# Kernel optimization log

Hardware: AMD Instinct MI355X
Metric: run time of the kernel (lower is better)

## Reference

```python
import jax, jax.numpy as jnp
import numpy as np

CONF = 0.25      # confidence threshold (module default)
IOU = 0.45       # NMS IoU threshold (class attribute)
TOPK = 1000      # fixed candidate budget (jit-friendly stand-in for boolean filtering)
MAX_WH = 4096.0  # class offset so NMS is per-class (YOLOv5 trick)


def xywh2xyxy(b):
    xy, wh = b[..., :2], b[..., 2:4]
    return jnp.concatenate([xy - wh * 0.5, xy + wh * 0.5], axis=-1)


def box_iou(a, b):
    # a: [K,4] xyxy, b: [K,4] xyxy -> [K,K]
    lt = jnp.maximum(a[:, None, :2], b[None, :, :2])
    rb = jnp.minimum(a[:, None, 2:], b[None, :, 2:])
    wh = jnp.clip(rb - lt, 0.0)
    inter = wh[..., 0] * wh[..., 1]
    area_a = (a[:, 2] - a[:, 0]) * (a[:, 3] - a[:, 1])
    area_b = (b[:, 2] - b[:, 0]) * (b[:, 3] - b[:, 1])
    return inter / (area_a[:, None] + area_b[None, :] - inter + 1e-9)


def nms_single(pred):
    # pred: [N, 5+C] = (xywh, obj, cls scores)
    boxes = xywh2xyxy(pred[:, :4])
    obj = pred[:, 4]
    cls = pred[:, 5:]
    cls_conf = jnp.max(cls, axis=-1)
    cls_id = jnp.argmax(cls, axis=-1)
    score = obj * cls_conf                       # conf = obj_conf * cls_conf
    masked = jnp.where(score > CONF, score, -1.0)
    top_scores, idx = jax.lax.top_k(masked, TOPK)  # sorted descending
    boxes_k = boxes[idx]                          # [K,4]
    cls_k = cls_id[idx].astype(boxes.dtype)       # [K]
    valid_k = top_scores > CONF                   # candidates passing threshold
    # per-class NMS via coordinate offset
    off = boxes_k + cls_k[:, None] * MAX_WH
    iou = box_iou(off, off)
    iou = iou * (1.0 - jnp.eye(TOPK, dtype=iou.dtype))  # ignore self-IoU
    # greedy suppression in descending score order
    def step(suppressed, i):
        keep_i = jnp.logical_and(jnp.logical_not(suppressed[i]), valid_k[i])
        suppressed = jnp.logical_or(suppressed, jnp.logical_and(keep_i, iou[i] > IOU))
        return suppressed, keep_i
    _, keep = jax.lax.scan(step, jnp.zeros(TOPK, dtype=bool), jnp.arange(TOPK))
    det = jnp.concatenate([boxes_k, top_scores[:, None], cls_k[:, None]], axis=-1)  # [K,6]
    return jnp.where(keep[:, None], det, 0.0)


def setup_inputs() -> dict:
    key = jax.random.key(0)
    x = jax.random.uniform(key, (8, 25200, 85), dtype=jnp.float32)
    return {"x": x}


def reference(x):
    # [B, K, 6] detections (xyxy, conf, cls); suppressed/invalid rows zeroed.
    return jax.vmap(nms_single)(x)
```

## Files before the change

### kernel.cpp

```cpp
#include <hip/hip_runtime.h>
#include <stdint.h>

#define NB 8
#define NPRED 25200
#define NTOP 1000
#define NCLS 80
#define CONF_T 0.25f
#define IOU_THR 0.45f
#define MAXWH 4096.0f
#define CAP 2048
#define NBINS 1025
#define SBLK 128
#define SBPB 197

typedef unsigned long long u64;

__device__ __forceinline__ u64 shfl_xor_u64(u64 v, int m) {
    int lo = __shfl_xor((int)(unsigned)v, m);
    int hi = __shfl_xor((int)(unsigned)(v >> 32), m);
    return ((u64)(unsigned)hi << 32) | (unsigned)lo;
}

__global__ __launch_bounds__(256) void k_score(const float* __restrict__ x,
                                               float* __restrict__ msc,
                                               int* __restrict__ cls) {
#pragma clang fp contract(off)
    __shared__ __align__(16) float sm[SBLK * 85];
    const int b = blockIdx.x / SBPB;
    const int blk = blockIdx.x % SBPB;
    const int t = threadIdx.x;
    const int wave = t >> 6, lane = t & 63;
    const long long TOT4 = (long long)NB * NPRED * 85 / 4;
    const long long base4 = ((long long)b * NPRED + (long long)blk * SBLK) * 85 / 4;
    const float4* x4 = (const float4*)x;
    const int tile4 = SBLK * 85 / 4;

    for (int k = 0; k < 11; ++k) {
        int ib = k * 256 + wave * 64;
        int fi = ib + lane;
        if (fi < tile4) {
            long long gi = base4 + fi;
            if (gi >= TOT4) gi = TOT4 - 1;
            __builtin_amdgcn_global_load_lds(
                (const __attribute__((address_space(1))) void*)(x4 + gi),
                (__attribute__((address_space(3))) void*)(sm + (size_t)ib * 4),
                16, 0, 0);
        }
    }
    __syncthreads();

    const int p = t >> 1;
    const int h = t & 1;
    const int pred = blk * SBLK + p;
    const float* rowp = &sm[p * 85];
    float obj = rowp[4];
    const int cb = 5 + h * 40;
    float best = rowp[cb];
    int bid = h * 40;
    for (int c = 1; c < 40; ++c) {
        float v = rowp[cb + c];
        if (v > best) { best = v; bid = h * 40 + c; }
    }
    float obest = __shfl_xor(best, 1);
    int obid = __shfl_xor(bid, 1);
    if (h == 0 && pred < NPRED) {
        float fb = best; int fc = bid;
        if (obest > fb) { fb = obest; fc = obid; }
        float score = obj * fb;
        int q = b * NPRED + pred;
        msc[q] = (score > CONF_T) ? score : -1.0f;
        cls[q] = fc;
    }
}

__global__ __launch_bounds__(1024) void k_fused(const float* __restrict__ x,
                                                const float* __restrict__ msc,
                                                const int* __restrict__ cls,
                                                float* __restrict__ out) {
#pragma clang fp contract(off)
    __shared__ __align__(16) unsigned char uni[CAP * 8];
    __shared__ unsigned hh[NBINS];
    __shared__ __align__(16) float4 obx[NTOP];
    __shared__ float oco[NTOP];
    __shared__ float osc[NTOP];
    __shared__ int   ocl[NTOP];
    __shared__ int sB;
    __shared__ unsigned lcnt;
    __shared__ int ovf;
    u64* keys = (u64*)uni;
    const int b = blockIdx.x, t = threadIdx.x;
    const float* ms = msc + (size_t)b * NPRED;

    float sv[25];
#pragma unroll
    for (int k = 0; k < 25; ++k) {
        int p = t + k * 1024;
        sv[k] = (p < NPRED) ? ms[p] : -1.0f;
    }

    for (int i = t; i < NBINS; i += 1024) hh[i] = 0;
    if (t == 0) { lcnt = 0; ovf = 0; }
    __syncthreads();

#pragma unroll
    for (int k = 0; k < 25; ++k) {
        float s = sv[k];
        if (s > CONF_T) {
            unsigned bits = __float_as_uint(s);
            int bin = (int)(bits >> 14) - 0xFA00;
            bin = bin < 0 ? 0 : (bin > 1024 ? 1024 : bin);
            atomicAdd(&hh[bin], 1u);
        }
    }
    __syncthreads();

    if (t < 64) {
        const int lane = t;
        const int hi2 = 1024 - 16 * lane;
        unsigned sum = 0;
        for (int k = 0; k < 16; ++k) sum += hh[hi2 - k];
        if (lane == 63) sum += hh[0];
        unsigned v = sum;
        for (int d = 1; d < 64; d <<= 1) {
            unsigned o = __shfl_up(v, d);
            if (lane >= d) v += o;
        }
        unsigned excl = v - sum;
        u64 ball = __ballot(v >= NTOP);
        int B = 0;
        if (ball != 0) {
            int sel = __builtin_ctzll(ball);
            if (lane == sel) {
                unsigned run = excl;
                for (int k = 0; k < 16; ++k) {
                    run += hh[hi2 - k];
                    if (run >= NTOP) { B = hi2 - k; break; }
                }
            }
            B = __shfl(B, sel);
        }
        if (lane == 0) sB = B;
    }
    __syncthreads();
    const int B = sB;

#pragma unroll
    for (int k = 0; k < 25; ++k) {
        float s = sv[k];
        if (s > CONF_T) {
            unsigned bits = __float_as_uint(s);
            int bin = (int)(bits >> 14) - 0xFA00;
            bin = bin < 0 ? 0 : (bin > 1024 ? 1024 : bin);
            if (bin >= B) {
                unsigned slot = atomicAdd(&lcnt, 1u);
                if (slot < CAP)
                    keys[slot] = ((u64)(~bits) << 32) | (unsigned)(t + k * 1024);
            }
        }
    }
    __syncthreads();
    unsigned c = lcnt; if (c > CAP) c = CAP;
    for (int i = (int)c + t; i < CAP; i += 1024) keys[i] = ~0ULL;
    __syncthreads();

    const unsigned ia = (((unsigned)t & ~63u) << 1) | ((unsigned)t & 63u);
    const unsigned ib = ia + 64u;

    auto ce = [&](u64& v, unsigned i, unsigned j, unsigned k) {
        u64 pv = shfl_xor_u64(v, (int)j);
        bool asc = ((i & k) == 0u);
        bool lower = ((i & j) == 0u);
        bool takeMin = (asc == lower);
        bool less = (v < pv);
        v = (takeMin == less) ? v : pv;
    };

    {
        u64 a = keys[ia], d = keys[ib];
        for (unsigned k = 2; k <= 64; k <<= 1)
            for (unsigned j = k >> 1; j >= 1; j >>= 1) {
                ce(a, ia, j, k);
                ce(d, ib, j, k);
            }
        keys[ia] = a; keys[ib] = d;
    }
    __syncthreads();

    for (unsigned k = 128; k <= CAP; k <<= 1) {
        for (unsigned j = k >> 1; j >= 64; j >>= 1) {
            unsigned i = (((unsigned)t & ~(j - 1)) << 1) | ((unsigned)t & (j - 1));
            unsigned pi = i | j;
            bool up = ((i & k) == 0);
            u64 a = keys[i], d = keys[pi];
            bool sw = up ? (a > d) : (a < d);
            if (sw) { keys[i] = d; keys[pi] = a; }
            __syncthreads();
        }
        u64 a = keys[ia], d = keys[ib];
        for (unsigned j = 32; j >= 1; j >>= 1) {
            ce(a, ia, j, k);
            ce(d, ib, j, k);
        }
        keys[ia] = a; keys[ib] = d;
        __syncthreads();
    }

    if (t < NTOP) {
        u64 key = keys[t];
        unsigned p = (unsigned)key;
        float score = __uint_as_float(~(unsigned)(key >> 32));
        bool v = score > CONF_T;
        float4 o = make_float4(0.f, 0.f, 0.f, 0.f);
        float co = 0.f; int cid = -1;
        if (v) {
            const float* xp = x + ((size_t)b * NPRED + p) * 85;
            float xc = xp[0], yc = xp[1], w = xp[2], h = xp[3];
            float hw = w * 0.5f, hh2 = h * 0.5f;
            o.x = xc - hw; o.y = yc - hh2; o.z = xc + hw; o.w = yc + hh2;
            cid = cls[(size_t)b * NPRED + p];
            co = (float)cid * MAXWH;
        }
        obx[t] = o; oco[t] = co; osc[t] = score; ocl[t] = cid;
    }
    __syncthreads();

    unsigned* keys32 = (unsigned*)uni;
    int* clsStart = (int*)(uni + 4096);
    int* clsEnd = (int*)(uni + 4416);
    unsigned char* sup = uni + 4736;

    unsigned v32 = (t < NTOP && ocl[t] >= 0)
                       ? (((unsigned)ocl[t] << 10) | (unsigned)t) : 0xFFFFFFFFu;

    auto ce32 = [&](unsigned& v, unsigned j, unsigned k) {
        unsigned pv = (unsigned)__shfl_xor((int)v, (int)j);
        bool asc = (((unsigned)t & k) == 0u);
        bool lower = (((unsigned)t & j) == 0u);
        bool takeMin = (asc == lower);
        v = ((v < pv) == takeMin) ? v : pv;
    };

    for (unsigned k = 2; k <= 64; k <<= 1)
        for (unsigned j = k >> 1; j >= 1; j >>= 1) ce32(v32, j, k);

    for (unsigned k = 128; k <= 1024; k <<= 1) {
        for (unsigned j = k >> 1; j >= 64; j >>= 1) {
            keys32[t] = v32;
            __syncthreads();
            unsigned pv = keys32[t ^ j];
            bool asc = (((unsigned)t & k) == 0u);
            bool lower = (((unsigned)t & j) == 0u);
            bool takeMin = (asc == lower);
            v32 = ((v32 < pv) == takeMin) ? v32 : pv;
            __syncthreads();
        }
        for (unsigned j = 32; j >= 1; j >>= 1) ce32(v32, j, k);
    }
    if (t < NTOP) sup[t] = 0;
    if (t < NCLS) { clsStart[t] = 0; clsEnd[t] = 0; }
    keys32[t] = v32;
    __syncthreads();

    {
        unsigned kk = keys32[t];
        if (kk != 0xFFFFFFFFu) {
            int c2 = (int)(kk >> 10);
            unsigned prev = (t > 0) ? keys32[t - 1] : 0xFFFFFFFFu;
            if (t == 0 || (int)(prev >> 10) != c2) clsStart[c2] = t;
            unsigned nxt = (t < 1023) ? keys32[t + 1] : 0xFFFFFFFFu;
            if (t == 1023 || (int)(nxt >> 10) != c2) clsEnd[c2] = t + 1;
        }
    }
    __syncthreads();

    {
        const int waveId = t >> 6, lane2 = t & 63;
        for (int c2 = waveId; c2 < NCLS; c2 += 16) {
            int s2 = clsStart[c2];
            int n2 = clsEnd[c2] - s2;
            if (n2 <= 0) continue;
            if (n2 > 64) { ovf = 1; continue; }
            int rank = 0;
            float ax1v = 0.f, ay1v = 0.f, ax2v = 0.f, ay2v = 0.f, arv = 0.f;
            if (lane2 < n2) {
                rank = (int)(keys32[s2 + lane2] & 1023u);
                float4 A = obx[rank]; float cA = oco[rank];
                ax1v = A.x + cA; ay1v = A.y + cA;
                ax2v = A.z + cA; ay2v = A.w + cA;
                arv = (ax2v - ax1v) * (ay2v - ay1v);
            }
            u64 alive = (n2 >= 64) ? ~0ull : ((1ull << n2) - 1ull);
            u64 kept = 0;
            while (alive) {
                int i = (int)__builtin_ctzll(alive);
                u64 bit = 1ull << i;
                kept |= bit;
                float bx1 = __shfl(ax1v, i), by1 = __shfl(ay1v, i);
                float bx2 = __shfl(ax2v, i), by2 = __shfl(ay2v, i);
                float bar = __shfl(arv, i);
                float ltx = fmaxf(bx1, ax1v), lty = fmaxf(by1, ay1v);
                float rbx = fminf(bx2, ax2v), rby = fminf(by2, ay2v);
                float ww = fmaxf(rbx - ltx, 0.0f), hh3 = fmaxf(rby - lty, 0.0f);
                float inter = ww * hh3;
                float iou = inter / (((bar + arv) - inter) + 1e-9f);
                u64 suppr = __ballot(iou > IOU_THR);
                alive &= ~(suppr | bit);
            }
            if (lane2 < n2) sup[rank] = ((kept >> lane2) & 1ull) ? 0 : 1;
        }
    }
    __syncthreads();

    if (ovf && t == 0) {
        for (int c2 = 0; c2 < NCLS; ++c2) {
            int s2 = clsStart[c2], e2 = clsEnd[c2];
            if (e2 - s2 <= 64) continue;
            for (int a2 = s2; a2 < e2; ++a2) {
                int ra = (int)(keys32[a2] & 1023u);
                if (sup[ra]) continue;
                float4 A = obx[ra]; float cA = oco[ra];
                float ax1 = A.x + cA, ay1 = A.y + cA;
                float ax2 = A.z + cA, ay2 = A.w + cA;
                float areaA = (ax2 - ax1) * (ay2 - ay1);
                for (int d2 = a2 + 1; d2 < e2; ++d2) {
                    int rd = (int)(keys32[d2] & 1023u);
                    if (sup[rd]) continue;
                    float4 Bb = obx[rd];
                    float bx1 = Bb.x + cA, by1 = Bb.y + cA;
                    float bx2 = Bb.z + cA, by2 = Bb.w + cA;
                    float ltx = fmaxf(ax1, bx1), lty = fmaxf(ay1, by1);
                    float rbx = fminf(ax2, bx2), rby = fminf(ay2, by2);
                    float ww = fmaxf(rbx - ltx, 0.0f), hh3 = fmaxf(rby - lty, 0.0f);
                    float inter = ww * hh3;
                    float areaB = (bx2 - bx1) * (by2 - by1);
                    float iou = inter / (((areaA + areaB) - inter) + 1e-9f);
                    if (iou > IOU_THR) sup[rd] = 1;
                }
            }
        }
    }
    __syncthreads();

    if (t < NTOP) {
        bool keep = (ocl[t] >= 0) && (sup[t] == 0);
        float4 o = obx[t];
        size_t d6 = ((size_t)b * NTOP + t) * 6;
        out[d6 + 0] = keep ? o.x : 0.0f;
        out[d6 + 1] = keep ? o.y : 0.0f;
        out[d6 + 2] = keep ? o.z : 0.0f;
        out[d6 + 3] = keep ? o.w : 0.0f;
        out[d6 + 4] = keep ? osc[t] : 0.0f;
        out[d6 + 5] = keep ? (float)ocl[t] : 0.0f;
    }
}

extern "C" void kernel_launch(void* const* d_in, const int* in_sizes, int n_in,
                              void* d_out, int out_size, void* d_ws, size_t ws_size,
                              hipStream_t stream) {
    const float* x = (const float*)d_in[0];
    char* ws = (char*)d_ws;
    float* msc = (float*)(ws);
    int* cls = (int*)(ws + 806400);

    k_score<<<NB * SBPB, 256, 0, stream>>>(x, msc, cls);
    k_fused<<<NB, 1024, 0, stream>>>(x, msc, cls, (float*)d_out);
}
```

Baseline: 134.8 us.

## Refine top-k histogram, add 1024-key sort path, replace class sort with bitmaps

The score histogram goes from 1025 to 8192 bins, with a two-level prefix scan, so the threshold bin is tighter and fewer candidates survive the cut. When at most 1024 keys survive, a one-key-per-thread bitonic sort over 1024 elements replaces the 2048-element sort. The per-class bitonic sort and start/end scan are replaced by per-class 64-bit membership bitmaps built with atomicOr, and each wave finds its members by popcount-based select. This removes several sort stages and barriers, in exchange for a larger shared histogram and more atomics into it.

```diff
diff --git a/kernel.cpp b/kernel.cpp
--- a/kernel.cpp
+++ b/kernel.cpp
@@ -9,7 +9,7 @@
 #define IOU_THR 0.45f
 #define MAXWH 4096.0f
 #define CAP 2048
-#define NBINS 1025
+#define NBINS2 8192
 #define SBLK 128
 #define SBPB 197
 
@@ -18,6 +18,11 @@
 __device__ __forceinline__ u64 shfl_xor_u64(u64 v, int m) {
     int lo = __shfl_xor((int)(unsigned)v, m);
     int hi = __shfl_xor((int)(unsigned)(v >> 32), m);
+    return ((u64)(unsigned)hi << 32) | (unsigned)lo;
+}
+__device__ __forceinline__ u64 shfl_u64(u64 v, int src) {
+    int lo = __shfl((int)(unsigned)v, src);
+    int hi = __shfl((int)(unsigned)(v >> 32), src);
     return ((u64)(unsigned)hi << 32) | (unsigned)lo;
 }
 
@@ -79,7 +84,7 @@
                                                 float* __restrict__ out) {
 #pragma clang fp contract(off)
     __shared__ __align__(16) unsigned char uni[CAP * 8];
-    __shared__ unsigned hh[NBINS];
+    __shared__ __align__(16) unsigned hh[NBINS2];
     __shared__ __align__(16) float4 obx[NTOP];
     __shared__ float oco[NTOP];
     __shared__ float osc[NTOP];
@@ -98,8 +103,8 @@
         sv[k] = (p < NPRED) ? ms[p] : -1.0f;
     }
 
-    for (int i = t; i < NBINS; i += 1024) hh[i] = 0;
-    if (t == 0) { lcnt = 0; ovf = 0; }
+    for (int i = t; i < NBINS2; i += 1024) hh[i] = 0;
+    if (t == 0) { lcnt = 0; ovf = 0; sB = 0; }
     __syncthreads();
 
 #pragma unroll
@@ -107,19 +112,28 @@
         float s = sv[k];
         if (s > CONF_T) {
             unsigned bits = __float_as_uint(s);
-            int bin = (int)(bits >> 14) - 0xFA00;
-            bin = bin < 0 ? 0 : (bin > 1024 ? 1024 : bin);
+            int bin = (int)(bits >> 11) - 0x7D000;
+            bin = bin < 0 ? 0 : (bin > 8191 ? 8191 : bin);
             atomicAdd(&hh[bin], 1u);
         }
+    }
+    __syncthreads();
+
+    unsigned* ctmp = (unsigned*)uni;
+    {
+        const uint4* h4 = (const uint4*)hh;
+        uint4 a = h4[t * 2], d = h4[t * 2 + 1];
+        ctmp[t] = a.x + a.y + a.z + a.w + d.x + d.y + d.z + d.w;
     }
     __syncthreads();
 
     if (t < 64) {
         const int lane = t;
-        const int hi2 = 1024 - 16 * lane;
+        const int hi = 1023 - 16 * lane;
+        unsigned lc[16];
         unsigned sum = 0;
-        for (int k = 0; k < 16; ++k) sum += hh[hi2 - k];
-        if (lane == 63) sum += hh[0];
+#pragma unroll
+        for (int k = 0; k < 16; ++k) { lc[k] = ctmp[hi - k]; sum += lc[k]; }
         unsigned v = sum;
         for (int d = 1; d < 64; d <<= 1) {
             unsigned o = __shfl_up(v, d);
@@ -127,19 +141,28 @@
         }
         unsigned excl = v - sum;
         u64 ball = __ballot(v >= NTOP);
-        int B = 0;
         if (ball != 0) {
             int sel = __builtin_ctzll(ball);
             if (lane == sel) {
-                unsigned run = excl;
+                unsigned run = excl, runBefore = 0;
+                int C = 0;
                 for (int k = 0; k < 16; ++k) {
-                    run += hh[hi2 - k];
-                    if (run >= NTOP) { B = hi2 - k; break; }
-                }
-            }
-            B = __shfl(B, sel);
-        }
-        if (lane == 0) sB = B;
+                    runBefore = run;
+                    run += lc[k];
+                    if (run >= NTOP) { C = hi - k; break; }
+                }
+                const uint4* f4 = (const uint4*)&hh[C * 8];
+                uint4 fa = f4[0], fb = f4[1];
+                unsigned fbin[8] = {fa.x, fa.y, fa.z, fa.w, fb.x, fb.y, fb.z, fb.w};
+                unsigned run2 = runBefore;
+                int Bf = C * 8;
+                for (int ff = 7; ff >= 0; --ff) {
+                    run2 += fbin[ff];
+                    if (run2 >= NTOP) { Bf = C * 8 + ff; break; }
+                }
+                sB = Bf;
+            }
+        }
     }
     __syncthreads();
     const int B = sB;
@@ -149,8 +172,8 @@
         float s = sv[k];
         if (s > CONF_T) {
             unsigned bits = __float_as_uint(s);
-            int bin = (int)(bits >> 14) - 0xFA00;
-            bin = bin < 0 ? 0 : (bin > 1024 ? 1024 : bin);
+            int bin = (int)(bits >> 11) - 0x7D000;
+            bin = bin < 0 ? 0 : (bin > 8191 ? 8191 : bin);
             if (bin >= B) {
                 unsigned slot = atomicAdd(&lcnt, 1u);
                 if (slot < CAP)
@@ -160,49 +183,81 @@
     }
     __syncthreads();
     unsigned c = lcnt; if (c > CAP) c = CAP;
-    for (int i = (int)c + t; i < CAP; i += 1024) keys[i] = ~0ULL;
-    __syncthreads();
-
-    const unsigned ia = (((unsigned)t & ~63u) << 1) | ((unsigned)t & 63u);
-    const unsigned ib = ia + 64u;
-
-    auto ce = [&](u64& v, unsigned i, unsigned j, unsigned k) {
-        u64 pv = shfl_xor_u64(v, (int)j);
-        bool asc = ((i & k) == 0u);
-        bool lower = ((i & j) == 0u);
-        bool takeMin = (asc == lower);
-        bool less = (v < pv);
-        v = (takeMin == less) ? v : pv;
-    };
-
-    {
-        u64 a = keys[ia], d = keys[ib];
+    const bool fastSort = (c <= 1024u);
+    const unsigned PAD = fastSort ? 1024u : (unsigned)CAP;
+    for (unsigned i = c + t; i < PAD; i += 1024) keys[i] = ~0ULL;
+    __syncthreads();
+
+    if (fastSort) {
+        u64 v = keys[t];
         for (unsigned k = 2; k <= 64; k <<= 1)
             for (unsigned j = k >> 1; j >= 1; j >>= 1) {
+                u64 pv = shfl_xor_u64(v, (int)j);
+                bool asc = (((unsigned)t & k) == 0u);
+                bool lower = (((unsigned)t & j) == 0u);
+                bool tm = (asc == lower);
+                v = ((v < pv) == tm) ? v : pv;
+            }
+        for (unsigned k = 128; k <= 1024; k <<= 1) {
+            for (unsigned j = k >> 1; j >= 64; j >>= 1) {
+                keys[t] = v;
+                __syncthreads();
+                u64 pv = keys[(unsigned)t ^ j];
+                bool asc = (((unsigned)t & k) == 0u);
+                bool lower = (((unsigned)t & j) == 0u);
+                bool tm = (asc == lower);
+                v = ((v < pv) == tm) ? v : pv;
+                __syncthreads();
+            }
+            for (unsigned j = 32; j >= 1; j >>= 1) {
+                u64 pv = shfl_xor_u64(v, (int)j);
+                bool asc = (((unsigned)t & k) == 0u);
+                bool lower = (((unsigned)t & j) == 0u);
+                bool tm = (asc == lower);
+                v = ((v < pv) == tm) ? v : pv;
+            }
+        }
+        keys[t] = v;
+        __syncthreads();
+    } else {
+        const unsigned ia = (((unsigned)t & ~63u) << 1) | ((unsigned)t & 63u);
+        const unsigned ib = ia + 64u;
+        auto ce = [&](u64& v, unsigned i, unsigned j, unsigned k) {
+            u64 pv = shfl_xor_u64(v, (int)j);
+            bool asc = ((i & k) == 0u);
+            bool lower = ((i & j) == 0u);
+            bool takeMin = (asc == lower);
+            bool less = (v < pv);
+            v = (takeMin == less) ? v : pv;
+        };
+        {
+            u64 a = keys[ia], d = keys[ib];
+            for (unsigned k = 2; k <= 64; k <<= 1)
+                for (unsigned j = k >> 1; j >= 1; j >>= 1) {
+                    ce(a, ia, j, k);
+                    ce(d, ib, j, k);
+                }
+            keys[ia] = a; keys[ib] = d;
+        }
+        __syncthreads();
+        for (unsigned k = 128; k <= CAP; k <<= 1) {
+            for (unsigned j = k >> 1; j >= 64; j >>= 1) {
+                unsigned i = (((unsigned)t & ~(j - 1)) << 1) | ((unsigned)t & (j - 1));
+                unsigned pi = i | j;
+                bool up = ((i & k) == 0);
+                u64 a = keys[i], d = keys[pi];
+                bool sw = up ? (a > d) : (a < d);
+                if (sw) { keys[i] = d; keys[pi] = a; }
+                __syncthreads();
+            }
+            u64 a = keys[ia], d = keys[ib];
+            for (unsigned j = 32; j >= 1; j >>= 1) {
                 ce(a, ia, j, k);
                 ce(d, ib, j, k);
             }
-        keys[ia] = a; keys[ib] = d;
-    }
-    __syncthreads();
-
-    for (unsigned k = 128; k <= CAP; k <<= 1) {
-        for (unsigned j = k >> 1; j >= 64; j >>= 1) {
-            unsigned i = (((unsigned)t & ~(j - 1)) << 1) | ((unsigned)t & (j - 1));
-            unsigned pi = i | j;
-            bool up = ((i & k) == 0);
-            u64 a = keys[i], d = keys[pi];
-            bool sw = up ? (a > d) : (a < d);
-            if (sw) { keys[i] = d; keys[pi] = a; }
+            keys[ia] = a; keys[ib] = d;
             __syncthreads();
         }
-        u64 a = keys[ia], d = keys[ib];
-        for (unsigned j = 32; j >= 1; j >>= 1) {
-            ce(a, ia, j, k);
-            ce(d, ib, j, k);
-        }
-        keys[ia] = a; keys[ib] = d;
-        __syncthreads();
     }
 
     if (t < NTOP) {
@@ -224,66 +279,43 @@
     }
     __syncthreads();
 
-    unsigned* keys32 = (unsigned*)uni;
-    int* clsStart = (int*)(uni + 4096);
-    int* clsEnd = (int*)(uni + 4416);
-    unsigned char* sup = uni + 4736;
-
-    unsigned v32 = (t < NTOP && ocl[t] >= 0)
-                       ? (((unsigned)ocl[t] << 10) | (unsigned)t) : 0xFFFFFFFFu;
-
-    auto ce32 = [&](unsigned& v, unsigned j, unsigned k) {
-        unsigned pv = (unsigned)__shfl_xor((int)v, (int)j);
-        bool asc = (((unsigned)t & k) == 0u);
-        bool lower = (((unsigned)t & j) == 0u);
-        bool takeMin = (asc == lower);
-        v = ((v < pv) == takeMin) ? v : pv;
-    };
-
-    for (unsigned k = 2; k <= 64; k <<= 1)
-        for (unsigned j = k >> 1; j >= 1; j >>= 1) ce32(v32, j, k);
-
-    for (unsigned k = 128; k <= 1024; k <<= 1) {
-        for (unsigned j = k >> 1; j >= 64; j >>= 1) {
-            keys32[t] = v32;
-            __syncthreads();
-            unsigned pv = keys32[t ^ j];
-            bool asc = (((unsigned)t & k) == 0u);
-            bool lower = (((unsigned)t & j) == 0u);
-            bool takeMin = (asc == lower);
-            v32 = ((v32 < pv) == takeMin) ? v32 : pv;
-            __syncthreads();
-        }
-        for (unsigned j = 32; j >= 1; j >>= 1) ce32(v32, j, k);
-    }
+    u64* bm = (u64*)uni;
+    unsigned char* sup = uni + 10240;
+    for (int i = t; i < NCLS * 16; i += 1024) bm[i] = 0;
     if (t < NTOP) sup[t] = 0;
-    if (t < NCLS) { clsStart[t] = 0; clsEnd[t] = 0; }
-    keys32[t] = v32;
-    __syncthreads();
-
-    {
-        unsigned kk = keys32[t];
-        if (kk != 0xFFFFFFFFu) {
-            int c2 = (int)(kk >> 10);
-            unsigned prev = (t > 0) ? keys32[t - 1] : 0xFFFFFFFFu;
-            if (t == 0 || (int)(prev >> 10) != c2) clsStart[c2] = t;
-            unsigned nxt = (t < 1023) ? keys32[t + 1] : 0xFFFFFFFFu;
-            if (t == 1023 || (int)(nxt >> 10) != c2) clsEnd[c2] = t + 1;
-        }
-    }
+    __syncthreads();
+    if (t < NTOP && ocl[t] >= 0)
+        atomicOr(&bm[ocl[t] * 16 + (t >> 6)], 1ull << (t & 63));
     __syncthreads();
 
     {
         const int waveId = t >> 6, lane2 = t & 63;
         for (int c2 = waveId; c2 < NCLS; c2 += 16) {
-            int s2 = clsStart[c2];
-            int n2 = clsEnd[c2] - s2;
-            if (n2 <= 0) continue;
+            u64 w = (lane2 < 16) ? bm[c2 * 16 + lane2] : 0ull;
+            int cum = 0, myw = -1, rem = 0;
+            u64 myword = 0;
+#pragma unroll
+            for (int ww = 0; ww < 16; ++ww) {
+                u64 wv = shfl_u64(w, ww);
+                int pc = __popcll(wv);
+                if (myw < 0 && lane2 < cum + pc) { myw = ww; rem = lane2 - cum; myword = wv; }
+                cum += pc;
+            }
+            int n2 = cum;
+            if (n2 == 0) continue;
             if (n2 > 64) { ovf = 1; continue; }
+            bool active = (lane2 < n2);
             int rank = 0;
             float ax1v = 0.f, ay1v = 0.f, ax2v = 0.f, ay2v = 0.f, arv = 0.f;
-            if (lane2 < n2) {
-                rank = (int)(keys32[s2 + lane2] & 1023u);
+            if (active) {
+                int pos = 0, r = rem;
+#pragma unroll
+                for (int wd = 32; wd >= 1; wd >>= 1) {
+                    u64 mask = ((1ull << wd) - 1ull) << pos;
+                    int cc = __popcll(myword & mask);
+                    if (r >= cc) { r -= cc; pos += wd; }
+                }
+                rank = myw * 64 + pos;
                 float4 A = obx[rank]; float cA = oco[rank];
                 ax1v = A.x + cA; ay1v = A.y + cA;
                 ax2v = A.z + cA; ay2v = A.w + cA;
@@ -300,32 +332,31 @@
                 float bar = __shfl(arv, i);
                 float ltx = fmaxf(bx1, ax1v), lty = fmaxf(by1, ay1v);
                 float rbx = fminf(bx2, ax2v), rby = fminf(by2, ay2v);
-                float ww = fmaxf(rbx - ltx, 0.0f), hh3 = fmaxf(rby - lty, 0.0f);
-                float inter = ww * hh3;
+                float ww2 = fmaxf(rbx - ltx, 0.0f), hh3 = fmaxf(rby - lty, 0.0f);
+                float inter = ww2 * hh3;
                 float iou = inter / (((bar + arv) - inter) + 1e-9f);
                 u64 suppr = __ballot(iou > IOU_THR);
                 alive &= ~(suppr | bit);
             }
-            if (lane2 < n2) sup[rank] = ((kept >> lane2) & 1ull) ? 0 : 1;
+            if (active) sup[rank] = ((kept >> lane2) & 1ull) ? 0 : 1;
         }
     }
     __syncthreads();
 
     if (ovf && t == 0) {
         for (int c2 = 0; c2 < NCLS; ++c2) {
-            int s2 = clsStart[c2], e2 = clsEnd[c2];
-            if (e2 - s2 <= 64) continue;
-            for (int a2 = s2; a2 < e2; ++a2) {
-                int ra = (int)(keys32[a2] & 1023u);
-                if (sup[ra]) continue;
-                float4 A = obx[ra]; float cA = oco[ra];
+            int n2 = 0;
+            for (int w2 = 0; w2 < 16; ++w2) n2 += __popcll(bm[c2 * 16 + w2]);
+            if (n2 <= 64) continue;
+            for (int a2 = 0; a2 < NTOP; ++a2) {
+                if (ocl[a2] != c2 || sup[a2]) continue;
+                float4 A = obx[a2]; float cA = oco[a2];
                 float ax1 = A.x + cA, ay1 = A.y + cA;
                 float ax2 = A.z + cA, ay2 = A.w + cA;
                 float areaA = (ax2 - ax1) * (ay2 - ay1);
-                for (int d2 = a2 + 1; d2 < e2; ++d2) {
-                    int rd = (int)(keys32[d2] & 1023u);
-                    if (sup[rd]) continue;
-                    float4 Bb = obx[rd];
+                for (int d2 = a2 + 1; d2 < NTOP; ++d2) {
+                    if (ocl[d2] != c2 || sup[d2]) continue;
+                    float4 Bb = obx[d2];
                     float bx1 = Bb.x + cA, by1 = Bb.y + cA;
                     float bx2 = Bb.z + cA, by2 = Bb.w + cA;
                     float ltx = fmaxf(ax1, bx1), lty = fmaxf(ay1, by1);
@@ -334,7 +365,7 @@
                     float inter = ww * hh3;
                     float areaB = (bx2 - bx1) * (by2 - by1);
                     float iou = inter / (((areaA + areaB) - inter) + 1e-9f);
-                    if (iou > IOU_THR) sup[rd] = 1;
+                    if (iou > IOU_THR) sup[d2] = 1;
                 }
             }
         }
```

New measurement: 134.0 us. About the same (-0.7%).
